# Optimization experiments

Hardware: AMD Instinct MI355X
Metric: run time of the kernel (lower is better)

Reference implementation:

```python
import jax, jax.numpy as jnp
import numpy as np

B, T, V, E, H, C, L = 32, 120, 32000, 256, 512, 20, 10
LN_EPS = 1e-5

# static span enumeration matching the original loop order:
# for begin in range(T): for span_len in 1..L if begin+span_len-1 < T
_begs, _lens = [], []
for _b in range(T):
    for _l in range(1, min(L, T - _b) + 1):
        _begs.append(_b); _lens.append(_l)
BEGS = np.asarray(_begs, np.int32)   # [S], S = 1155
LENS = np.asarray(_lens, np.int32)
S = len(_begs)


def setup_inputs() -> dict:
    key = jax.random.key(0)
    ks = jax.random.split(key, 12)
    rn = lambda k, shape, s=0.05: (jax.random.normal(k, shape, jnp.float32) * s)
    return {
        "tokens": jax.random.randint(ks[0], (B, T), 0, V, dtype=jnp.int32),
        "emb": rn(ks[1], (V, E)),
        "w_ih_f": rn(ks[2], (4 * H, E)), "w_hh_f": rn(ks[3], (4 * H, H)),
        "b_ih_f": jnp.zeros((4 * H,), jnp.float32), "b_hh_f": jnp.zeros((4 * H,), jnp.float32),
        "w_ih_b": rn(ks[4], (4 * H, E)), "w_hh_b": rn(ks[5], (4 * H, H)),
        "b_ih_b": jnp.zeros((4 * H,), jnp.float32), "b_hh_b": jnp.zeros((4 * H,), jnp.float32),
        "lin1_w": rn(ks[6], (H, 2 * H)), "lin1_b": jnp.zeros((H,), jnp.float32),
        "lin2_w": rn(ks[7], (H, H)), "lin2_b": jnp.zeros((H,), jnp.float32),
        "ln_g": jnp.ones((H,), jnp.float32), "ln_b": jnp.zeros((H,), jnp.float32),
        "label_w": rn(ks[8], (H, C)), "label_b": rn(ks[9], (C,)),
    }


def _lstm_dir(x, w_ih, w_hh, b_ih, b_hh, reverse):
    # x: [B, T, E] -> hs: [B, T, H]; torch gate order i, f, g, o
    xs = jnp.swapaxes(x, 0, 1)          # [T, B, E]
    if reverse:
        xs = xs[::-1]
    xg = xs @ w_ih.T + (b_ih + b_hh)    # [T, B, 4H] input contribution precomputed
    h0 = jnp.zeros((x.shape[0], w_hh.shape[1]), x.dtype)

    def step(carry, g_in):
        h, c = carry
        g = g_in + h @ w_hh.T
        i, f, gg, o = jnp.split(g, 4, axis=-1)
        c = jax.nn.sigmoid(f) * c + jax.nn.sigmoid(i) * jnp.tanh(gg)
        h = jax.nn.sigmoid(o) * jnp.tanh(c)
        return (h, c), h

    _, hs = jax.lax.scan(step, (h0, h0), xg)
    if reverse:
        hs = hs[::-1]
    return jnp.swapaxes(hs, 0, 1)


def reference(tokens, emb, w_ih_f, w_hh_f, b_ih_f, b_hh_f,
              w_ih_b, w_hh_b, b_ih_b, b_hh_b,
              lin1_w, lin1_b, lin2_w, lin2_b, ln_g, ln_b,
              label_w, label_b):
    x = emb[tokens]                                          # [B, T, E]
    fwd = _lstm_dir(x, w_ih_f, w_hh_f, b_ih_f, b_hh_f, False)
    bwd = _lstm_dir(x, w_ih_b, w_hh_b, b_ih_b, b_hh_b, True)
    rnn_out = jnp.concatenate([fwd, bwd], axis=-1)           # [B, T, 2H]

    # non_linear: Linear -> Dropout(eval: identity) -> ReLU -> Linear -> LayerNorm
    h = jax.nn.relu(rnn_out @ lin1_w.T + lin1_b)
    h = h @ lin2_w.T + lin2_b
    mu = jnp.mean(h, axis=-1, keepdims=True)
    var = jnp.var(h, axis=-1, keepdims=True)
    token_repr = (h - mu) / jnp.sqrt(var + LN_EPS) * ln_g + ln_b  # [B, T, H]

    # span mean pooling via exclusive cumsum: mean over [beg, beg+len)
    cs = jnp.concatenate(
        [jnp.zeros_like(token_repr[:, :1]), jnp.cumsum(token_repr, axis=1)], axis=1)  # [B, T+1, H]
    begs = jnp.asarray(BEGS)
    ends = jnp.asarray(BEGS + LENS)
    inv_len = 1.0 / jnp.asarray(LENS, token_repr.dtype)[:, None]
    spans = (cs[:, ends] - cs[:, begs]) * inv_len            # [B, S, H]
    span_reprs = spans.reshape(-1, spans.shape[-1])          # [B*S, H], bid-major order

    score = jax.nn.log_softmax(span_reprs @ label_w + label_b, axis=0)
    return score
```

## Files before the change

### kernel.cpp

```cpp
#include <hip/hip_runtime.h>

#define B_ 32
#define T_ 120
#define E_ 256
#define H_ 512
#define NSPAN 36960

typedef __attribute__((ext_vector_type(8))) short short8;
typedef __attribute__((ext_vector_type(4))) short sshort4;
typedef __attribute__((ext_vector_type(4))) float f32x4;
typedef __attribute__((ext_vector_type(4))) unsigned int u32x4;

__device__ __forceinline__ short f2bf(float x) {
    union { float f; unsigned u; } v; v.f = x;
    unsigned r = v.u + 0x7fffu + ((v.u >> 16) & 1u);
    return (short)(r >> 16);
}
__device__ __forceinline__ float bf2f(unsigned short x) {
    union { unsigned u; float f; } v; v.u = ((unsigned)x) << 16;
    return v.f;
}
__device__ __forceinline__ int load_coh_i32(const int* p) {
    int r;
    asm volatile("global_load_dword %0, %1, off sc0 sc1\n\ts_waitcnt vmcnt(0)"
                 : "=v"(r) : "v"(p) : "memory");
    return r;
}

__global__ void k_gather(const int* __restrict__ tokens, const float* __restrict__ emb,
                         short* __restrict__ xbf) {
    int m = blockIdx.x;
    int t = m >> 5, b = m & 31;
    int tok = tokens[b * T_ + t];
    int e = threadIdx.x;
    xbf[(size_t)m * E_ + e] = f2bf(emb[(size_t)tok * E_ + e]);
}

__global__ void k_convert(const float* __restrict__ src, short* __restrict__ dst, int n8) {
    int i = blockIdx.x * blockDim.x + threadIdx.x;
    if (i >= n8) return;
    const float4* s4 = (const float4*)src + (size_t)i * 2;
    float4 a = s4[0], b = s4[1];
    short8 o;
    o[0]=f2bf(a.x); o[1]=f2bf(a.y); o[2]=f2bf(a.z); o[3]=f2bf(a.w);
    o[4]=f2bf(b.x); o[5]=f2bf(b.y); o[6]=f2bf(b.z); o[7]=f2bf(b.w);
    *(short8*)(dst + (size_t)i * 8) = o;
}

__global__ void k_biascomb(const float* __restrict__ bf1, const float* __restrict__ bf2,
                           const float* __restrict__ bb1, const float* __restrict__ bb2,
                           float* __restrict__ out) {
    int i = blockIdx.x * 256 + threadIdx.x;
    out[i] = (i < 2048) ? (bf1[i] + bf2[i]) : (bb1[i - 2048] + bb2[i - 2048]);
}

template <int EPI>
__global__ void __launch_bounds__(256) k_gemm(const short* __restrict__ A,
                                              const short* __restrict__ W,
                                              const float* __restrict__ bias,
                                              float* __restrict__ outF,
                                              short* __restrict__ outB,
                                              int N, int K) {
    int w = threadIdx.x >> 6, l = threadIdx.x & 63;
    int la = l & 15, lb = l >> 4;
    int m0 = blockIdx.x * 64 + w * 16;
    int nb = blockIdx.y * 64;
    const short* Ap = A + (size_t)(m0 + la) * K + lb * 8;
    const short* Wp = W + (size_t)(nb + la) * K + lb * 8;
    f32x4 acc0 = {0.f,0.f,0.f,0.f}, acc1 = acc0, acc2 = acc0, acc3 = acc0;
    for (int k0 = 0; k0 < K; k0 += 32) {
        short8 a  = *(const short8*)(Ap + k0);
        short8 b0 = *(const short8*)(Wp + k0);
        short8 b1 = *(const short8*)(Wp + (size_t)16 * K + k0);
        short8 b2 = *(const short8*)(Wp + (size_t)32 * K + k0);
        short8 b3 = *(const short8*)(Wp + (size_t)48 * K + k0);
        acc0 = __builtin_amdgcn_mfma_f32_16x16x32_bf16(a, b0, acc0, 0, 0, 0);
        acc1 = __builtin_amdgcn_mfma_f32_16x16x32_bf16(a, b1, acc1, 0, 0, 0);
        acc2 = __builtin_amdgcn_mfma_f32_16x16x32_bf16(a, b2, acc2, 0, 0, 0);
        acc3 = __builtin_amdgcn_mfma_f32_16x16x32_bf16(a, b3, acc3, 0, 0, 0);
    }
    f32x4 accs[4] = {acc0, acc1, acc2, acc3};
    #pragma unroll
    for (int j = 0; j < 4; ++j) {
        int n = nb + j * 16 + la;
        float bv = bias[n];
        if (EPI == 2) {
            int mb = m0 + lb * 4;
            int t = mb >> 5, b0i = mb & 31;
            sshort4 pk;
            #pragma unroll
            for (int r = 0; r < 4; ++r) pk[r] = f2bf(accs[j][r] + bv);
            *(sshort4*)(outB + (((size_t)t * 4096 + n) << 5) + b0i) = pk;
        } else {
            #pragma unroll
            for (int r = 0; r < 4; ++r) {
                int m = m0 + lb * 4 + r;
                float v = accs[j][r] + bv;
                if (EPI == 0) outF[(size_t)m * N + n] = v;
                else          outB[(size_t)m * N + n] = f2bf(fmaxf(v, 0.f));
            }
        }
    }
}

__global__ void __launch_bounds__(256, 1) k_lstm(const short* __restrict__ xg,
                                                 const short* __restrict__ whh,
                                                 short* __restrict__ hbuf,
                                                 short* __restrict__ rnn,
                                                 int* __restrict__ ctr) {
    __shared__ short wlds[4][16][512];
    __shared__ short hlds[32][512];
    int tid = threadIdx.x;
    int w = tid >> 6, l = tid & 63;
    int la = l & 15, lb = l >> 4;
    int bid = blockIdx.x;
    int dir = bid >> 5, jsl = bid & 31;
    int jw = jsl * 16 + w * 4;

    {
        char* base = (char*)&wlds[w][0][0];
        for (int cc = l; cc < 1024; cc += 64) {
            int rr = cc >> 6, c16 = cc & 63;
            int gate = rr >> 2, jj = rr & 3;
            short8 v = *(const short8*)(whh + ((size_t)dir * 2048 + gate * 512 + jw + jj) * 512 + c16 * 8);
            *(short8*)(base + rr * 1024 + ((c16 * 16) ^ ((rr & 7) << 4))) = v;
        }
    }
    __syncthreads();

    float cst[2][4] = {{0.f,0.f,0.f,0.f},{0.f,0.f,0.f,0.f}};
    int gate = la >> 2;
    int grow = dir * 2048 + gate * 512 + jw + (la & 3);
    const char* wrow = (const char*)&wlds[w][0][0] + la * 1024;
    const char* hrow0 = (const char*)&hlds[0][0] + la * 1024;
    const char* hrow1 = hrow0 + 16 * 1024;
    int swz = (la & 7) << 4;
    int* ctrd = ctr + dir * T_;

    for (int s = 0; s < T_; ++s) {
        int t = dir ? (T_ - 1 - s) : s;
        int cur = s & 1;
        const short* hb = hbuf + (size_t)(dir * 2 + cur) * (32 * 512);
        short* hn = hbuf + (size_t)(dir * 2 + (1 - cur)) * (32 * 512);

        if (s > 0) {
            if (tid == 0) {
                const int* cp = ctrd + (s - 1);
                while (load_coh_i32(cp) < 32) __builtin_amdgcn_s_sleep(1);
            }
            __syncthreads();
        }

        unsigned long long x0, x1;
        {
            u32x4 vv[8];
            const char* src = (const char*)hb;
            #pragma unroll
            for (int i = 0; i < 8; ++i)
                asm volatile("global_load_dwordx4 %0, %1, off sc0 sc1"
                             : "=v"(vv[i]) : "v"(src + (tid + 256 * i) * 16));
            const short* xgp = xg + ((size_t)t * 4096 + grow) * 32;
            x0 = *(const unsigned long long*)(xgp + lb * 4);
            x1 = *(const unsigned long long*)(xgp + 16 + lb * 4);
            asm volatile("s_waitcnt vmcnt(0)" ::: "memory");
            char* hdst = (char*)&hlds[0][0];
            #pragma unroll
            for (int i = 0; i < 8; ++i) {
                int byte = (tid + 256 * i) << 4;
                int row = byte >> 10, col = byte & 1023;
                *(u32x4*)(hdst + row * 1024 + (col ^ ((row & 7) << 4))) = vv[i];
            }
        }
        __syncthreads();

        float xv[2][4];
        #pragma unroll
        for (int r = 0; r < 4; ++r) {
            xv[0][r] = bf2f((unsigned short)((x0 >> (16 * r)) & 0xffffu));
            xv[1][r] = bf2f((unsigned short)((x1 >> (16 * r)) & 0xffffu));
        }

        f32x4 a0A = {0.f,0.f,0.f,0.f}, a0B = a0A, a1A = a0A, a1B = a0A;
        #pragma unroll
        for (int ks2 = 0; ks2 < 8; ++ks2) {
            int co0 = ((ks2 * 128) + lb * 16) ^ swz;
            int co1 = co0 ^ 64;
            short8 wA = *(const short8*)(wrow + co0);
            short8 wB = *(const short8*)(wrow + co1);
            short8 h0A = *(const short8*)(hrow0 + co0);
            short8 h0B = *(const short8*)(hrow0 + co1);
            short8 h1A = *(const short8*)(hrow1 + co0);
            short8 h1B = *(const short8*)(hrow1 + co1);
            a0A = __builtin_amdgcn_mfma_f32_16x16x32_bf16(h0A, wA, a0A, 0, 0, 0);
            a1A = __builtin_amdgcn_mfma_f32_16x16x32_bf16(h1A, wA, a1A, 0, 0, 0);
            a0B = __builtin_amdgcn_mfma_f32_16x16x32_bf16(h0B, wB, a0B, 0, 0, 0);
            a1B = __builtin_amdgcn_mfma_f32_16x16x32_bf16(h1B, wB, a1B, 0, 0, 0);
        }
        f32x4 a0 = a0A + a0B, a1 = a1A + a1B;

        float val[2][4];
        #pragma unroll
        for (int mt = 0; mt < 2; ++mt) {
            #pragma unroll
            for (int r = 0; r < 4; ++r) {
                float x = (mt ? a1[r] : a0[r]) + xv[mt][r];
                val[mt][r] = (gate == 2) ? (1.f - 2.f / (1.f + __expf(2.f * x)))
                                         : (1.f / (1.f + __expf(-x)));
            }
        }

        #pragma unroll
        for (int mt = 0; mt < 2; ++mt) {
            #pragma unroll
            for (int r = 0; r < 4; ++r) {
                float v = val[mt][r];
                float vf = __shfl_xor(v, 4);
                float vg = __shfl_xor(v, 8);
                float vo = __shfl_xor(v, 12);
                if (la < 4) {
                    float c = vf * cst[mt][r] + v * vg;
                    cst[mt][r] = c;
                    float h = vo * (1.f - 2.f / (1.f + __expf(2.f * c)));
                    short hv = f2bf(h);
                    int hvi = (unsigned short)hv;
                    int b = mt * 16 + lb * 4 + r;
                    asm volatile("global_store_short %0, %1, off sc0 sc1"
                                 :: "v"(hn + (size_t)b * 512 + jw + la), "v"(hvi) : "memory");
                    rnn[((size_t)b * T_ + t) * 1024 + dir * 512 + jw + la] = hv;
                }
            }
        }

        asm volatile("s_waitcnt vmcnt(0)" ::: "memory");
        __syncthreads();
        if (tid == 0)
            __hip_atomic_fetch_add(ctrd + s, 1, __ATOMIC_RELAXED, __HIP_MEMORY_SCOPE_AGENT);
    }
}

__global__ void k_ln(const float* __restrict__ h2, const float* __restrict__ gam,
                     const float* __restrict__ bet, float* __restrict__ tr) {
    int w = threadIdx.x >> 6, l = threadIdx.x & 63;
    size_t row = (size_t)blockIdx.x * 4 + w;
    const float* x = h2 + row * 512;
    float v[8], s = 0.f, s2 = 0.f;
    #pragma unroll
    for (int i = 0; i < 8; ++i) { v[i] = x[l + 64 * i]; s += v[i]; s2 += v[i] * v[i]; }
    #pragma unroll
    for (int off = 32; off; off >>= 1) { s += __shfl_xor(s, off); s2 += __shfl_xor(s2, off); }
    float mu = s * (1.f / 512.f);
    float var = s2 * (1.f / 512.f) - mu * mu;
    float rstd = 1.f / sqrtf(var + 1e-5f);
    float* o = tr + row * 512;
    #pragma unroll
    for (int i = 0; i < 8; ++i) { int k = l + 64 * i; o[k] = (v[i] - mu) * rstd * gam[k] + bet[k]; }
}

__global__ void k_cumsum(const float* __restrict__ tr, float* __restrict__ cs) {
    int b = blockIdx.x, f = threadIdx.x;
    cs[((size_t)b * 121) * 512 + f] = 0.f;
    const float* src = tr + ((size_t)b * 120) * 512 + f;
    float* dst = cs + ((size_t)b * 121 + 1) * 512 + f;
    float run = 0.f;
    float nxt = src[0];
    for (int t = 0; t < 120; ++t) {
        float c = nxt;
        if (t < 119) nxt = src[(size_t)(t + 1) * 512];
        run += c;
        dst[(size_t)t * 512] = run;
    }
}

__global__ void __launch_bounds__(256) k_span(const float* __restrict__ cs,
                                              const float* __restrict__ lw,
                                              const float* __restrict__ lbias,
                                              float* __restrict__ out) {
    __shared__ float wl[20][512];
    for (int idx = threadIdx.x; idx < 20 * 512; idx += 256) {
        int c = idx >> 9, k = idx & 511;
        wl[c][k] = lw[(size_t)k * 20 + c];
    }
    __syncthreads();
    int w = threadIdx.x >> 6, l = threadIdx.x & 63;
    int nw = gridDim.x * 4;
    for (int sp = blockIdx.x * 4 + w; sp < NSPAN; sp += nw) {
        int b = sp / 1155, s = sp - b * 1155;
        int beg, len;
        if (s < 1110) { beg = s / 10; len = s - beg * 10 + 1; }
        else {
            int t2 = s - 1110; beg = 111; int ll = 9;
            while (t2 >= ll) { t2 -= ll; --ll; ++beg; }
            len = t2 + 1;
        }
        int end = beg + len;
        const float* ce = cs + ((size_t)b * 121 + end) * 512;
        const float* cb = cs + ((size_t)b * 121 + beg) * 512;
        float inv = 1.f / (float)len;
        float p[20];
        #pragma unroll
        for (int c = 0; c < 20; ++c) p[c] = 0.f;
        #pragma unroll
        for (int i = 0; i < 8; ++i) {
            int k = l + 64 * i;
            float d = (ce[k] - cb[k]) * inv;
            #pragma unroll
            for (int c = 0; c < 20; ++c) p[c] += d * wl[c][k];
        }
        #pragma unroll
        for (int off = 32; off; off >>= 1) {
            #pragma unroll
            for (int c = 0; c < 20; ++c) p[c] += __shfl_xor(p[c], off);
        }
        if (l == 0) {
            float* o = out + (size_t)sp * 20;
            #pragma unroll
            for (int c = 0; c < 20; ++c) o[c] = p[c] + lbias[c];
        }
    }
}

__global__ void __launch_bounds__(256) k_lsepart(const float* __restrict__ logits,
                                                 float2* __restrict__ part) {
    float m[20], sm[20];
    #pragma unroll
    for (int c = 0; c < 20; ++c) { m[c] = -1e30f; sm[c] = 0.f; }
    for (int row = blockIdx.x * 256 + threadIdx.x; row < NSPAN; row += gridDim.x * 256) {
        const float* r = logits + (size_t)row * 20;
        #pragma unroll
        for (int c = 0; c < 20; ++c) {
            float x = r[c];
            float nm = fmaxf(m[c], x);
            sm[c] = sm[c] * expf(m[c] - nm) + expf(x - nm);
            m[c] = nm;
        }
    }
    __shared__ float2 red[256][20];
    #pragma unroll
    for (int c = 0; c < 20; ++c) red[threadIdx.x][c] = make_float2(m[c], sm[c]);
    __syncthreads();
    for (int st = 128; st; st >>= 1) {
        if (threadIdx.x < st) {
            #pragma unroll
            for (int c = 0; c < 20; ++c) {
                float2 a = red[threadIdx.x][c], b = red[threadIdx.x + st][c];
                float nm = fmaxf(a.x, b.x);
                float ss = a.y * expf(a.x - nm) + b.y * expf(b.x - nm);
                red[threadIdx.x][c] = make_float2(nm, ss);
            }
        }
        __syncthreads();
    }
    if (threadIdx.x < 20) part[(size_t)blockIdx.x * 20 + threadIdx.x] = red[0][threadIdx.x];
}

__global__ void k_lsefin(const float2* __restrict__ part, int nparts, float* __restrict__ lse) {
    int c = threadIdx.x;
    if (c >= 20) return;
    float m = -1e30f, s = 0.f;
    for (int i = 0; i < nparts; ++i) {
        float2 a = part[(size_t)i * 20 + c];
        float nm = fmaxf(m, a.x);
        s = s * expf(m - nm) + a.y * expf(a.x - nm);
        m = nm;
    }
    lse[c] = m + logf(s);
}

__global__ void k_sub(float* __restrict__ out, const float* __restrict__ lse) {
    int i = blockIdx.x * 256 + threadIdx.x;
    if (i < NSPAN * 20) out[i] -= lse[i % 20];
}

extern "C" void kernel_launch(void* const* d_in, const int* in_sizes, int n_in,
                              void* d_out, int out_size, void* d_ws, size_t ws_size,
                              hipStream_t stream) {
    (void)in_sizes; (void)n_in; (void)out_size; (void)ws_size;
    const int*   tokens = (const int*)  d_in[0];
    const float* emb    = (const float*)d_in[1];
    const float* w_ih_f = (const float*)d_in[2];
    const float* w_hh_f = (const float*)d_in[3];
    const float* b_ih_f = (const float*)d_in[4];
    const float* b_hh_f = (const float*)d_in[5];
    const float* w_ih_b = (const float*)d_in[6];
    const float* w_hh_b = (const float*)d_in[7];
    const float* b_ih_b = (const float*)d_in[8];
    const float* b_hh_b = (const float*)d_in[9];
    const float* lin1_w = (const float*)d_in[10];
    const float* lin1_b = (const float*)d_in[11];
    const float* lin2_w = (const float*)d_in[12];
    const float* lin2_b = (const float*)d_in[13];
    const float* ln_g   = (const float*)d_in[14];
    const float* ln_b   = (const float*)d_in[15];
    const float* label_w= (const float*)d_in[16];
    const float* label_b= (const float*)d_in[17];
    float* out = (float*)d_out;

    char* ws = (char*)d_ws;
    size_t off = 0;
    auto alloc = [&](size_t bytes) { char* p = ws + off; off += (bytes + 255) & ~size_t(255); return p; };
    short*  xbf   = (short*)alloc(3840ull * 256 * 2);
    short*  wihbf = (short*)alloc(4096ull * 256 * 2);
    short*  whhbf = (short*)alloc(2ull * 2048 * 512 * 2);
    short*  l1wbf = (short*)alloc(512ull * 1024 * 2);
    short*  l2wbf = (short*)alloc(512ull * 512 * 2);
    float*  biasc = (float*)alloc(4096ull * 4);
    short*  xg    = (short*)alloc(120ull * 4096 * 32 * 2);
    short*  hbuf  = (short*)alloc(4ull * 32 * 512 * 2);
    short*  rnn   = (short*)alloc(3840ull * 1024 * 2);
    short*  h1    = (short*)alloc(3840ull * 512 * 2);
    float*  h2    = (float*)alloc(3840ull * 512 * 4);
    float*  tr    = (float*)alloc(3840ull * 512 * 4);
    float*  cs    = (float*)alloc(32ull * 121 * 512 * 4);
    int*    ctr   = (int*)  alloc(1024);
    float2* part  = (float2*)alloc(120ull * 20 * 8);
    float*  lse   = (float*)alloc(256);

    hipMemsetAsync(hbuf, 0, 4ull * 32 * 512 * 2, stream);
    hipMemsetAsync(ctr, 0, 1024, stream);

    k_gather<<<3840, 256, 0, stream>>>(tokens, emb, xbf);
    int n8;
    n8 = 2048 * 256 / 8; k_convert<<<(n8 + 255) / 256, 256, 0, stream>>>(w_ih_f, wihbf, n8);
    n8 = 2048 * 256 / 8; k_convert<<<(n8 + 255) / 256, 256, 0, stream>>>(w_ih_b, wihbf + 2048ull * 256, n8);
    n8 = 2048 * 512 / 8; k_convert<<<(n8 + 255) / 256, 256, 0, stream>>>(w_hh_f, whhbf, n8);
    n8 = 2048 * 512 / 8; k_convert<<<(n8 + 255) / 256, 256, 0, stream>>>(w_hh_b, whhbf + 2048ull * 512, n8);
    n8 = 512 * 1024 / 8; k_convert<<<(n8 + 255) / 256, 256, 0, stream>>>(lin1_w, l1wbf, n8);
    n8 = 512 * 512 / 8;  k_convert<<<(n8 + 255) / 256, 256, 0, stream>>>(lin2_w, l2wbf, n8);
    k_biascomb<<<16, 256, 0, stream>>>(b_ih_f, b_hh_f, b_ih_b, b_hh_b, biasc);

    k_gemm<2><<<dim3(60, 64), 256, 0, stream>>>(xbf, wihbf, biasc, nullptr, xg, 4096, 256);
    k_lstm<<<64, 256, 0, stream>>>(xg, whhbf, hbuf, rnn, ctr);
    k_gemm<1><<<dim3(60, 8), 256, 0, stream>>>(rnn, l1wbf, lin1_b, nullptr, h1, 512, 1024);
    k_gemm<0><<<dim3(60, 8), 256, 0, stream>>>(h1, l2wbf, lin2_b, h2, nullptr, 512, 512);
    k_ln<<<960, 256, 0, stream>>>(h2, ln_g, ln_b, tr);
    k_cumsum<<<32, 512, 0, stream>>>(tr, cs);
    k_span<<<512, 256, 0, stream>>>(cs, label_w, label_b, out);
    k_lsepart<<<120, 256, 0, stream>>>(out, part);
    k_lsefin<<<1, 32, 0, stream>>>(part, 120, lse);
    k_sub<<<(NSPAN * 20 + 255) / 256, 256, 0, stream>>>(out, lse);
}
```

Before: 850.2 us.

## Replace LSTM counter barrier with per-step sentinel-polled hidden-state buffers

The recurrent kernel no longer uses a global atomic counter, spin-wait and block barriers between timesteps. Each step now writes to its own slot in a buffer pre-filled with 0xFF and polls that slot for non-sentinel data, so MFMA work can start on whichever chunks have already arrived. W_hh is held in registers instead of LDS, and h is packed through a small LDS tile into 8-byte stores. It also unrolls the cumsum load loop and aliases later buffers onto dead workspace. Risks are correctness if a real bf16 pair ever equals the all-ones sentinel, a bounded-retry exit that can read stale data, and higher register pressure from 16 short8 weight fragments.

```diff
diff --git a/kernel.cpp b/kernel.cpp
--- a/kernel.cpp
+++ b/kernel.cpp
@@ -10,6 +10,7 @@
 typedef __attribute__((ext_vector_type(4))) short sshort4;
 typedef __attribute__((ext_vector_type(4))) float f32x4;
 typedef __attribute__((ext_vector_type(4))) unsigned int u32x4;
+typedef unsigned long long ull;
 
 __device__ __forceinline__ short f2bf(float x) {
     union { float f; unsigned u; } v; v.f = x;
@@ -20,12 +21,12 @@
     union { unsigned u; float f; } v; v.u = ((unsigned)x) << 16;
     return v.f;
 }
-__device__ __forceinline__ int load_coh_i32(const int* p) {
-    int r;
-    asm volatile("global_load_dword %0, %1, off sc0 sc1\n\ts_waitcnt vmcnt(0)"
-                 : "=v"(r) : "v"(p) : "memory");
-    return r;
-}
+
+#define LDX4(dst, base, OFFS) \
+    asm volatile("global_load_dwordx4 %0, %1, off offset:" OFFS " sc0 sc1" \
+                 : "=v"(dst) : "v"(base))
+#define RETRY2(ks, OFFS) \
+    if (need & (1u << ks)) { LDX4(hr0[ks], hb0, OFFS); LDX4(hr1[ks], hb1, OFFS); }
 
 __global__ void k_gather(const int* __restrict__ tokens, const float* __restrict__ emb,
                          short* __restrict__ xbf) {
@@ -105,73 +106,54 @@
 
 __global__ void __launch_bounds__(256, 1) k_lstm(const short* __restrict__ xg,
                                                  const short* __restrict__ whh,
-                                                 short* __restrict__ hbuf,
-                                                 short* __restrict__ rnn,
-                                                 int* __restrict__ ctr) {
-    __shared__ short wlds[4][16][512];
-    __shared__ short hlds[32][512];
+                                                 const short* __restrict__ hzero,
+                                                 short* __restrict__ hsteps,
+                                                 short* __restrict__ rnn) {
+    __shared__ short hpack[4][32][4];
     int tid = threadIdx.x;
     int w = tid >> 6, l = tid & 63;
     int la = l & 15, lb = l >> 4;
     int bid = blockIdx.x;
     int dir = bid >> 5, jsl = bid & 31;
     int jw = jsl * 16 + w * 4;
-
+    int gate = la >> 2;
+    int row = dir * 2048 + gate * 512 + jw + (la & 3);
+
+    short8 wf[16];
     {
-        char* base = (char*)&wlds[w][0][0];
-        for (int cc = l; cc < 1024; cc += 64) {
-            int rr = cc >> 6, c16 = cc & 63;
-            int gate = rr >> 2, jj = rr & 3;
-            short8 v = *(const short8*)(whh + ((size_t)dir * 2048 + gate * 512 + jw + jj) * 512 + c16 * 8);
-            *(short8*)(base + rr * 1024 + ((c16 * 16) ^ ((rr & 7) << 4))) = v;
-        }
-    }
-    __syncthreads();
+        const short* wr = whh + (size_t)row * 512 + lb * 8;
+        #pragma unroll
+        for (int ks = 0; ks < 16; ++ks) wf[ks] = *(const short8*)(wr + ks * 32);
+    }
 
     float cst[2][4] = {{0.f,0.f,0.f,0.f},{0.f,0.f,0.f,0.f}};
-    int gate = la >> 2;
-    int grow = dir * 2048 + gate * 512 + jw + (la & 3);
-    const char* wrow = (const char*)&wlds[w][0][0] + la * 1024;
-    const char* hrow0 = (const char*)&hlds[0][0] + la * 1024;
-    const char* hrow1 = hrow0 + 16 * 1024;
-    int swz = (la & 7) << 4;
-    int* ctrd = ctr + dir * T_;
 
     for (int s = 0; s < T_; ++s) {
         int t = dir ? (T_ - 1 - s) : s;
-        int cur = s & 1;
-        const short* hb = hbuf + (size_t)(dir * 2 + cur) * (32 * 512);
-        short* hn = hbuf + (size_t)(dir * 2 + (1 - cur)) * (32 * 512);
-
-        if (s > 0) {
-            if (tid == 0) {
-                const int* cp = ctrd + (s - 1);
-                while (load_coh_i32(cp) < 32) __builtin_amdgcn_s_sleep(1);
-            }
-            __syncthreads();
-        }
-
-        unsigned long long x0, x1;
+        const short* hb = (s == 0) ? hzero
+                                   : (hsteps + ((size_t)(dir * T_ + (s - 1)) << 14));
+        short* hn = hsteps + ((size_t)(dir * T_ + s) << 14);
+        const short* hb0 = hb + la * 512 + lb * 8;
+        const short* hb1 = hb0 + 16 * 512;
+
+        ull x0, x1;
         {
-            u32x4 vv[8];
-            const char* src = (const char*)hb;
-            #pragma unroll
-            for (int i = 0; i < 8; ++i)
-                asm volatile("global_load_dwordx4 %0, %1, off sc0 sc1"
-                             : "=v"(vv[i]) : "v"(src + (tid + 256 * i) * 16));
-            const short* xgp = xg + ((size_t)t * 4096 + grow) * 32;
-            x0 = *(const unsigned long long*)(xgp + lb * 4);
-            x1 = *(const unsigned long long*)(xgp + 16 + lb * 4);
-            asm volatile("s_waitcnt vmcnt(0)" ::: "memory");
-            char* hdst = (char*)&hlds[0][0];
-            #pragma unroll
-            for (int i = 0; i < 8; ++i) {
-                int byte = (tid + 256 * i) << 4;
-                int row = byte >> 10, col = byte & 1023;
-                *(u32x4*)(hdst + row * 1024 + (col ^ ((row & 7) << 4))) = vv[i];
-            }
-        }
-        __syncthreads();
+            const short* xgp = xg + (size_t)t * 131072 + (size_t)row * 32 + lb * 4;
+            asm volatile("global_load_dwordx2 %0, %1, off" : "=v"(x0) : "v"(xgp));
+            asm volatile("global_load_dwordx2 %0, %1, off offset:32" : "=v"(x1) : "v"(xgp));
+        }
+
+        u32x4 hr0[16], hr1[16];
+        LDX4(hr0[0],hb0,"0");   LDX4(hr0[1],hb0,"64");  LDX4(hr0[2],hb0,"128"); LDX4(hr0[3],hb0,"192");
+        LDX4(hr0[4],hb0,"256"); LDX4(hr0[5],hb0,"320"); LDX4(hr0[6],hb0,"384"); LDX4(hr0[7],hb0,"448");
+        LDX4(hr0[8],hb0,"512"); LDX4(hr0[9],hb0,"576"); LDX4(hr0[10],hb0,"640");LDX4(hr0[11],hb0,"704");
+        LDX4(hr0[12],hb0,"768");LDX4(hr0[13],hb0,"832");LDX4(hr0[14],hb0,"896");LDX4(hr0[15],hb0,"960");
+        LDX4(hr1[0],hb1,"0");   LDX4(hr1[1],hb1,"64");  LDX4(hr1[2],hb1,"128"); LDX4(hr1[3],hb1,"192");
+        LDX4(hr1[4],hb1,"256"); LDX4(hr1[5],hb1,"320"); LDX4(hr1[6],hb1,"384"); LDX4(hr1[7],hb1,"448");
+        LDX4(hr1[8],hb1,"512"); LDX4(hr1[9],hb1,"576"); LDX4(hr1[10],hb1,"640");LDX4(hr1[11],hb1,"704");
+        LDX4(hr1[12],hb1,"768");LDX4(hr1[13],hb1,"832");LDX4(hr1[14],hb1,"896");LDX4(hr1[15],hb1,"960");
+        asm volatile("s_waitcnt vmcnt(0)" ::: "memory");
+        __builtin_amdgcn_sched_barrier(0);
 
         float xv[2][4];
         #pragma unroll
@@ -180,23 +162,42 @@
             xv[1][r] = bf2f((unsigned short)((x1 >> (16 * r)) & 0xffffu));
         }
 
-        f32x4 a0A = {0.f,0.f,0.f,0.f}, a0B = a0A, a1A = a0A, a1B = a0A;
-        #pragma unroll
-        for (int ks2 = 0; ks2 < 8; ++ks2) {
-            int co0 = ((ks2 * 128) + lb * 16) ^ swz;
-            int co1 = co0 ^ 64;
-            short8 wA = *(const short8*)(wrow + co0);
-            short8 wB = *(const short8*)(wrow + co1);
-            short8 h0A = *(const short8*)(hrow0 + co0);
-            short8 h0B = *(const short8*)(hrow0 + co1);
-            short8 h1A = *(const short8*)(hrow1 + co0);
-            short8 h1B = *(const short8*)(hrow1 + co1);
-            a0A = __builtin_amdgcn_mfma_f32_16x16x32_bf16(h0A, wA, a0A, 0, 0, 0);
-            a1A = __builtin_amdgcn_mfma_f32_16x16x32_bf16(h1A, wA, a1A, 0, 0, 0);
-            a0B = __builtin_amdgcn_mfma_f32_16x16x32_bf16(h0B, wB, a0B, 0, 0, 0);
-            a1B = __builtin_amdgcn_mfma_f32_16x16x32_bf16(h1B, wB, a1B, 0, 0, 0);
-        }
-        f32x4 a0 = a0A + a0B, a1 = a1A + a1B;
+        f32x4 ae0 = {0.f,0.f,0.f,0.f}, ao0 = ae0, ae1 = ae0, ao1 = ae0;
+        unsigned need = 0xFFFFu;
+        int tries = 0;
+        while (true) {
+            unsigned got = 0;
+            #pragma unroll
+            for (int ks = 0; ks < 16; ++ks) {
+                if (need & (1u << ks)) {
+                    u32x4 f0 = hr0[ks], f1 = hr1[ks];
+                    int bad = (f0[0] == 0xFFFFFFFFu) || (f0[2] == 0xFFFFFFFFu) ||
+                              (f1[0] == 0xFFFFFFFFu) || (f1[2] == 0xFFFFFFFFu);
+                    if (!__any(bad)) {
+                        short8 s0 = __builtin_bit_cast(short8, f0);
+                        short8 s1 = __builtin_bit_cast(short8, f1);
+                        if (ks & 1) {
+                            ao0 = __builtin_amdgcn_mfma_f32_16x16x32_bf16(s0, wf[ks], ao0, 0, 0, 0);
+                            ao1 = __builtin_amdgcn_mfma_f32_16x16x32_bf16(s1, wf[ks], ao1, 0, 0, 0);
+                        } else {
+                            ae0 = __builtin_amdgcn_mfma_f32_16x16x32_bf16(s0, wf[ks], ae0, 0, 0, 0);
+                            ae1 = __builtin_amdgcn_mfma_f32_16x16x32_bf16(s1, wf[ks], ae1, 0, 0, 0);
+                        }
+                        got |= 1u << ks;
+                    }
+                }
+            }
+            need &= ~got;
+            if (!need) break;
+            if (++tries > (1 << 17)) break;
+            RETRY2(0,"0");   RETRY2(1,"64");  RETRY2(2,"128"); RETRY2(3,"192");
+            RETRY2(4,"256"); RETRY2(5,"320"); RETRY2(6,"384"); RETRY2(7,"448");
+            RETRY2(8,"512"); RETRY2(9,"576"); RETRY2(10,"640");RETRY2(11,"704");
+            RETRY2(12,"768");RETRY2(13,"832");RETRY2(14,"896");RETRY2(15,"960");
+            asm volatile("s_waitcnt vmcnt(0)" ::: "memory");
+            __builtin_amdgcn_sched_barrier(0);
+        }
+        f32x4 a0 = ae0 + ao0, a1 = ae1 + ao1;
 
         float val[2][4];
         #pragma unroll
@@ -221,20 +222,18 @@
                     float c = vf * cst[mt][r] + v * vg;
                     cst[mt][r] = c;
                     float h = vo * (1.f - 2.f / (1.f + __expf(2.f * c)));
-                    short hv = f2bf(h);
-                    int hvi = (unsigned short)hv;
-                    int b = mt * 16 + lb * 4 + r;
-                    asm volatile("global_store_short %0, %1, off sc0 sc1"
-                                 :: "v"(hn + (size_t)b * 512 + jw + la), "v"(hvi) : "memory");
-                    rnn[((size_t)b * T_ + t) * 1024 + dir * 512 + jw + la] = hv;
+                    hpack[w][mt * 16 + lb * 4 + r][la] = f2bf(h);
                 }
             }
         }
-
-        asm volatile("s_waitcnt vmcnt(0)" ::: "memory");
-        __syncthreads();
-        if (tid == 0)
-            __hip_atomic_fetch_add(ctrd + s, 1, __ATOMIC_RELAXED, __HIP_MEMORY_SCOPE_AGENT);
+        __builtin_amdgcn_wave_barrier();
+        if (l < 32) {
+            ull pk = *(const ull*)&hpack[w][l][0];
+            short* hp = hn + (size_t)l * 512 + jw;
+            asm volatile("global_store_dwordx2 %0, %1, off sc0 sc1" :: "v"(hp), "v"(pk) : "memory");
+            *(ull*)(rnn + ((size_t)l * T_ + t) * 1024 + dir * 512 + jw) = pk;
+        }
+        __builtin_amdgcn_wave_barrier();
     }
 }
 
@@ -262,12 +261,12 @@
     const float* src = tr + ((size_t)b * 120) * 512 + f;
     float* dst = cs + ((size_t)b * 121 + 1) * 512 + f;
     float run = 0.f;
-    float nxt = src[0];
-    for (int t = 0; t < 120; ++t) {
-        float c = nxt;
-        if (t < 119) nxt = src[(size_t)(t + 1) * 512];
-        run += c;
-        dst[(size_t)t * 512] = run;
+    for (int t0 = 0; t0 < 120; t0 += 8) {
+        float v[8];
+        #pragma unroll
+        for (int i = 0; i < 8; ++i) v[i] = src[(size_t)(t0 + i) * 512];
+        #pragma unroll
+        for (int i = 0; i < 8; ++i) { run += v[i]; dst[(size_t)(t0 + i) * 512] = run; }
     }
 }
 
@@ -405,18 +404,18 @@
     short*  l2wbf = (short*)alloc(512ull * 512 * 2);
     float*  biasc = (float*)alloc(4096ull * 4);
     short*  xg    = (short*)alloc(120ull * 4096 * 32 * 2);
-    short*  hbuf  = (short*)alloc(4ull * 32 * 512 * 2);
+    short*  hzero = (short*)alloc(32ull * 512 * 2);
+    short*  hsteps= (short*)alloc(2ull * 120 * 32 * 512 * 2);
     short*  rnn   = (short*)alloc(3840ull * 1024 * 2);
-    short*  h1    = (short*)alloc(3840ull * 512 * 2);
-    float*  h2    = (float*)alloc(3840ull * 512 * 4);
-    float*  tr    = (float*)alloc(3840ull * 512 * 4);
-    float*  cs    = (float*)alloc(32ull * 121 * 512 * 4);
-    int*    ctr   = (int*)  alloc(1024);
     float2* part  = (float2*)alloc(120ull * 20 * 8);
     float*  lse   = (float*)alloc(256);
-
-    hipMemsetAsync(hbuf, 0, 4ull * 32 * 512 * 2, stream);
-    hipMemsetAsync(ctr, 0, 1024, stream);
+    short*  h1    = (short*)whhbf;
+    float*  h2    = (float*)hsteps;
+    float*  tr    = (float*)xg;
+    float*  cs    = (float*)((char*)xg + 8ull * 1024 * 1024);
+
+    hipMemsetAsync(hzero, 0x00, 32ull * 512 * 2, stream);
+    hipMemsetAsync(hsteps, 0xFF, 2ull * 120 * 32 * 512 * 2, stream);
 
     k_gather<<<3840, 256, 0, stream>>>(tokens, emb, xbf);
     int n8;
@@ -429,7 +428,7 @@
     k_biascomb<<<16, 256, 0, stream>>>(b_ih_f, b_hh_f, b_ih_b, b_hh_b, biasc);
 
     k_gemm<2><<<dim3(60, 64), 256, 0, stream>>>(xbf, wihbf, biasc, nullptr, xg, 4096, 256);
-    k_lstm<<<64, 256, 0, stream>>>(xg, whhbf, hbuf, rnn, ctr);
+    k_lstm<<<64, 256, 0, stream>>>(xg, whhbf, hzero, hsteps, rnn);
     k_gemm<1><<<dim3(60, 8), 256, 0, stream>>>(rnn, l1wbf, lin1_b, nullptr, h1, 512, 1024);
     k_gemm<0><<<dim3(60, 8), 256, 0, stream>>>(h1, l2wbf, lin2_b, h2, nullptr, 512, 512);
     k_ln<<<960, 256, 0, stream>>>(h2, ln_g, ln_b, tr);
```

Result: slower. 1.500 ms (+76.4%).

## Replace LSTM counter barrier with sentinel-polled per-step hidden buffers

Applied to the files above, without the earlier changes.

The cross-block LSTM step barrier (atomic counter plus spin by thread 0 and two block syncs) is replaced by per-timestep hidden-state buffers pre-filled with 0xFF. Consumers poll the loaded data itself until no sentinel words remain. Hidden outputs are staged in LDS and written as packed 8-byte stores instead of scattered short stores. The cumsum loop is batched by 8, and workspace buffers are aliased to fit the larger step buffer. This risks a false sentinel match on genuine bf16 pairs (NaN pattern) and adds a large memset.

```diff
diff --git a/kernel.cpp b/kernel.cpp
--- a/kernel.cpp
+++ b/kernel.cpp
@@ -10,6 +10,7 @@
 typedef __attribute__((ext_vector_type(4))) short sshort4;
 typedef __attribute__((ext_vector_type(4))) float f32x4;
 typedef __attribute__((ext_vector_type(4))) unsigned int u32x4;
+typedef unsigned long long ull;
 
 __device__ __forceinline__ short f2bf(float x) {
     union { float f; unsigned u; } v; v.f = x;
@@ -20,12 +21,9 @@
     union { unsigned u; float f; } v; v.u = ((unsigned)x) << 16;
     return v.f;
 }
-__device__ __forceinline__ int load_coh_i32(const int* p) {
-    int r;
-    asm volatile("global_load_dword %0, %1, off sc0 sc1\n\ts_waitcnt vmcnt(0)"
-                 : "=v"(r) : "v"(p) : "memory");
-    return r;
-}
+
+#define LDC(dst, addr) \
+    asm volatile("global_load_dwordx4 %0, %1, off sc0 sc1" : "=v"(dst) : "v"(addr))
 
 __global__ void k_gather(const int* __restrict__ tokens, const float* __restrict__ emb,
                          short* __restrict__ xbf) {
@@ -105,11 +103,12 @@
 
 __global__ void __launch_bounds__(256, 1) k_lstm(const short* __restrict__ xg,
                                                  const short* __restrict__ whh,
-                                                 short* __restrict__ hbuf,
-                                                 short* __restrict__ rnn,
-                                                 int* __restrict__ ctr) {
+                                                 const short* __restrict__ hzero,
+                                                 short* __restrict__ hsteps,
+                                                 short* __restrict__ rnn) {
     __shared__ short wlds[4][16][512];
     __shared__ short hlds[32][512];
+    __shared__ short hpack[4][32][4];
     int tid = threadIdx.x;
     int w = tid >> 6, l = tid & 63;
     int la = l & 15, lb = l >> 4;
@@ -135,34 +134,39 @@
     const char* hrow0 = (const char*)&hlds[0][0] + la * 1024;
     const char* hrow1 = hrow0 + 16 * 1024;
     int swz = (la & 7) << 4;
-    int* ctrd = ctr + dir * T_;
 
     for (int s = 0; s < T_; ++s) {
         int t = dir ? (T_ - 1 - s) : s;
-        int cur = s & 1;
-        const short* hb = hbuf + (size_t)(dir * 2 + cur) * (32 * 512);
-        short* hn = hbuf + (size_t)(dir * 2 + (1 - cur)) * (32 * 512);
-
-        if (s > 0) {
-            if (tid == 0) {
-                const int* cp = ctrd + (s - 1);
-                while (load_coh_i32(cp) < 32) __builtin_amdgcn_s_sleep(1);
-            }
-            __syncthreads();
-        }
-
-        unsigned long long x0, x1;
+        const short* hb = (s == 0) ? hzero
+                                   : (hsteps + ((size_t)(dir * T_ + (s - 1)) << 14));
+        short* hn = hsteps + ((size_t)(dir * T_ + s) << 14);
+
+        ull x0, x1;
         {
             u32x4 vv[8];
             const char* src = (const char*)hb;
             #pragma unroll
             for (int i = 0; i < 8; ++i)
-                asm volatile("global_load_dwordx4 %0, %1, off sc0 sc1"
-                             : "=v"(vv[i]) : "v"(src + (tid + 256 * i) * 16));
+                LDC(vv[i], src + (tid + 256 * i) * 16);
             const short* xgp = xg + ((size_t)t * 4096 + grow) * 32;
-            x0 = *(const unsigned long long*)(xgp + lb * 4);
-            x1 = *(const unsigned long long*)(xgp + 16 + lb * 4);
+            x0 = *(const ull*)(xgp + lb * 4);
+            x1 = *(const ull*)(xgp + 16 + lb * 4);
             asm volatile("s_waitcnt vmcnt(0)" ::: "memory");
+            __builtin_amdgcn_sched_barrier(0);
+            int tries = 0;
+            while (true) {
+                unsigned bad = 0;
+                #pragma unroll
+                for (int i = 0; i < 8; ++i)
+                    if (vv[i][0] == 0xFFFFFFFFu || vv[i][2] == 0xFFFFFFFFu) bad |= 1u << i;
+                if (!__any(bad != 0)) break;
+                if (++tries > (1 << 17)) break;
+                #pragma unroll
+                for (int i = 0; i < 8; ++i)
+                    if (bad & (1u << i)) LDC(vv[i], src + (tid + 256 * i) * 16);
+                asm volatile("s_waitcnt vmcnt(0)" ::: "memory");
+                __builtin_amdgcn_sched_barrier(0);
+            }
             char* hdst = (char*)&hlds[0][0];
             #pragma unroll
             for (int i = 0; i < 8; ++i) {
@@ -196,6 +200,7 @@
             a0B = __builtin_amdgcn_mfma_f32_16x16x32_bf16(h0B, wB, a0B, 0, 0, 0);
             a1B = __builtin_amdgcn_mfma_f32_16x16x32_bf16(h1B, wB, a1B, 0, 0, 0);
         }
+        __syncthreads();
         f32x4 a0 = a0A + a0B, a1 = a1A + a1B;
 
         float val[2][4];
@@ -221,20 +226,21 @@
                     float c = vf * cst[mt][r] + v * vg;
                     cst[mt][r] = c;
                     float h = vo * (1.f - 2.f / (1.f + __expf(2.f * c)));
-                    short hv = f2bf(h);
-                    int hvi = (unsigned short)hv;
-                    int b = mt * 16 + lb * 4 + r;
-                    asm volatile("global_store_short %0, %1, off sc0 sc1"
-                                 :: "v"(hn + (size_t)b * 512 + jw + la), "v"(hvi) : "memory");
-                    rnn[((size_t)b * T_ + t) * 1024 + dir * 512 + jw + la] = hv;
+                    hpack[w][mt * 16 + lb * 4 + r][la] = f2bf(h);
                 }
             }
         }
-
-        asm volatile("s_waitcnt vmcnt(0)" ::: "memory");
-        __syncthreads();
-        if (tid == 0)
-            __hip_atomic_fetch_add(ctrd + s, 1, __ATOMIC_RELAXED, __HIP_MEMORY_SCOPE_AGENT);
+        asm volatile("s_waitcnt lgkmcnt(0)" ::: "memory");
+        __builtin_amdgcn_sched_barrier(0);
+        __builtin_amdgcn_wave_barrier();
+
+        if (l < 32) {
+            ull pk = *(const ull*)&hpack[w][l][0];
+            short* hp = hn + (size_t)l * 512 + jw;
+            asm volatile("global_store_dwordx2 %0, %1, off sc0 sc1" :: "v"(hp), "v"(pk) : "memory");
+            *(ull*)(rnn + ((size_t)l * T_ + t) * 1024 + dir * 512 + jw) = pk;
+        }
+        __builtin_amdgcn_wave_barrier();
     }
 }
 
@@ -262,12 +268,12 @@
     const float* src = tr + ((size_t)b * 120) * 512 + f;
     float* dst = cs + ((size_t)b * 121 + 1) * 512 + f;
     float run = 0.f;
-    float nxt = src[0];
-    for (int t = 0; t < 120; ++t) {
-        float c = nxt;
-        if (t < 119) nxt = src[(size_t)(t + 1) * 512];
-        run += c;
-        dst[(size_t)t * 512] = run;
+    for (int t0 = 0; t0 < 120; t0 += 8) {
+        float v[8];
+        #pragma unroll
+        for (int i = 0; i < 8; ++i) v[i] = src[(size_t)(t0 + i) * 512];
+        #pragma unroll
+        for (int i = 0; i < 8; ++i) { run += v[i]; dst[(size_t)(t0 + i) * 512] = run; }
     }
 }
 
@@ -405,18 +411,18 @@
     short*  l2wbf = (short*)alloc(512ull * 512 * 2);
     float*  biasc = (float*)alloc(4096ull * 4);
     short*  xg    = (short*)alloc(120ull * 4096 * 32 * 2);
-    short*  hbuf  = (short*)alloc(4ull * 32 * 512 * 2);
+    short*  hzero = (short*)alloc(32ull * 512 * 2);
+    short*  hsteps= (short*)alloc(2ull * 120 * 32 * 512 * 2);
     short*  rnn   = (short*)alloc(3840ull * 1024 * 2);
-    short*  h1    = (short*)alloc(3840ull * 512 * 2);
-    float*  h2    = (float*)alloc(3840ull * 512 * 4);
-    float*  tr    = (float*)alloc(3840ull * 512 * 4);
-    float*  cs    = (float*)alloc(32ull * 121 * 512 * 4);
-    int*    ctr   = (int*)  alloc(1024);
     float2* part  = (float2*)alloc(120ull * 20 * 8);
     float*  lse   = (float*)alloc(256);
-
-    hipMemsetAsync(hbuf, 0, 4ull * 32 * 512 * 2, stream);
-    hipMemsetAsync(ctr, 0, 1024, stream);
+    short*  h1    = (short*)whhbf;
+    float*  h2    = (float*)hsteps;
+    float*  tr    = (float*)xg;
+    float*  cs    = (float*)((char*)xg + 8ull * 1024 * 1024);
+
+    hipMemsetAsync(hzero, 0x00, 32ull * 512 * 2, stream);
+    hipMemsetAsync(hsteps, 0xFF, 2ull * 120 * 32 * 512 * 2, stream);
 
     k_gather<<<3840, 256, 0, stream>>>(tokens, emb, xbf);
     int n8;
@@ -429,7 +435,7 @@
     k_biascomb<<<16, 256, 0, stream>>>(b_ih_f, b_hh_f, b_ih_b, b_hh_b, biasc);
 
     k_gemm<2><<<dim3(60, 64), 256, 0, stream>>>(xbf, wihbf, biasc, nullptr, xg, 4096, 256);
-    k_lstm<<<64, 256, 0, stream>>>(xg, whhbf, hbuf, rnn, ctr);
+    k_lstm<<<64, 256, 0, stream>>>(xg, whhbf, hzero, hsteps, rnn);
     k_gemm<1><<<dim3(60, 8), 256, 0, stream>>>(rnn, l1wbf, lin1_b, nullptr, h1, 512, 1024);
     k_gemm<0><<<dim3(60, 8), 256, 0, stream>>>(h1, l2wbf, lin2_b, h2, nullptr, 512, 512);
     k_ln<<<960, 256, 0, stream>>>(h2, ln_g, ln_b, tr);
```

Result: slower. 937.4 us (+10.3%).
